# Optimization experiments

Measured on AMD Instinct MI355X. Metric: run time of the kernel, lower is better.

The kernel has to match this reference:

```python
import jax, jax.numpy as jnp
import numpy as np

B, S, D = 1, 2048, 2048
H, HKV, HD = 16, 8, 128
WINDOW = 1024
EPS = 1e-6
SCALE = HD ** -0.5


def _rope_tables(seq_len, head_dim, theta=10000.0):
    inv_freq = 1.0 / (theta ** (jnp.arange(0, head_dim, 2, dtype=jnp.float32) / head_dim))
    ang = jnp.arange(seq_len, dtype=jnp.float32)[:, None] * inv_freq[None, :]  # [S, hd/2]
    emb = jnp.concatenate([ang, ang], axis=-1)  # [S, hd]
    return jnp.cos(emb)[None], jnp.sin(emb)[None]  # [1, S, hd]


def setup_inputs() -> dict:
    key = jax.random.key(0)
    ks = jax.random.split(key, 8)
    cos, sin = _rope_tables(S, HD)
    return {
        "hidden_states": jax.random.normal(ks[0], (B, S, D), jnp.float32),
        "cos": jnp.broadcast_to(cos, (B, S, HD)),
        "sin": jnp.broadcast_to(sin, (B, S, HD)),
        "Wq": jax.random.normal(ks[1], (D, H * HD), jnp.float32) * (D ** -0.5),
        "Wk": jax.random.normal(ks[2], (D, HKV * HD), jnp.float32) * (D ** -0.5),
        "Wv": jax.random.normal(ks[3], (D, HKV * HD), jnp.float32) * (D ** -0.5),
        "Wo": jax.random.normal(ks[4], (H * HD, D), jnp.float32) * ((H * HD) ** -0.5),
        "q_scale": jax.random.uniform(ks[5], (HD,), jnp.float32, 0.5, 1.5),
        "k_scale": jax.random.uniform(ks[6], (HD,), jnp.float32, 0.5, 1.5),
    }


def _rms_norm(x, scale):
    # per-head RMSNorm over last dim, computed in fp32 (matches RMSNorm module)
    xf = x.astype(jnp.float32)
    var = jnp.mean(xf * xf, axis=-1, keepdims=True)
    return (xf * jax.lax.rsqrt(var + EPS) * scale).astype(x.dtype)


def _rotate_half(x):
    x1, x2 = x[..., : HD // 2], x[..., HD // 2 :]
    return jnp.concatenate([-x2, x1], axis=-1)


def _apply_rope(x, cos, sin):
    # cos/sin: [B,S,hd] -> [B,S,1,hd] (unsqueeze_dim=2)
    c, s = cos[:, :, None, :], sin[:, :, None, :]
    return x * c + _rotate_half(x) * s


def reference(hidden_states, cos, sin, Wq, Wk, Wv, Wo, q_scale, k_scale):
    b, s, _ = hidden_states.shape
    q = (hidden_states @ Wq).reshape(b, s, H, HD)
    k = (hidden_states @ Wk).reshape(b, s, HKV, HD)
    v = (hidden_states @ Wv).reshape(b, s, HKV, HD)
    q = _rms_norm(q, q_scale)
    k = _rms_norm(k, k_scale)
    q = _apply_rope(q, cos, sin)
    k = _apply_rope(k, cos, sin)
    # GQA: repeat kv heads to match query heads (groups are consecutive)
    g = H // HKV
    k = jnp.repeat(k, g, axis=2)  # [b, s, H, hd]
    v = jnp.repeat(v, g, axis=2)
    scores = jnp.einsum("bqhd,bkhd->bhqk", q, k) * SCALE  # [b,H,S,S]
    i = jnp.arange(s)[:, None]
    j = jnp.arange(s)[None, :]
    allowed = (j <= i) & (i - j <= WINDOW)  # causal + sliding window
    scores = jnp.where(allowed[None, None], scores, -jnp.inf)
    attn = jax.nn.softmax(scores, axis=-1)
    out = jnp.einsum("bhqk,bkhd->bqhd", attn, v).reshape(b, s, H * HD)
    return out @ Wo
```

## Files before the change

### kernel.cpp

```cpp
#include <hip/hip_runtime.h>
#include <hip/hip_bf16.h>
#include <cmath>


typedef __bf16 bf16x8 __attribute__((ext_vector_type(8)));
typedef float  f32x4  __attribute__((ext_vector_type(4)));

#define S_LEN    2048
#define NH       16
#define NKV      8
#define HDIM     128
#define WIN      1024
#define QK_SCALE_L2E 0.12751744595f
#define RMS_EPS  1e-6f

__device__ __forceinline__ void gld16(void* lds, const void* g) {
    __builtin_amdgcn_global_load_lds(
        (const __attribute__((address_space(1))) unsigned int*)g,
        (__attribute__((address_space(3))) unsigned int*)lds, 16, 0, 0);
}

__device__ __forceinline__ unsigned short f2bu(float x) {
    __hip_bfloat16 h = __float2bfloat16(x);
    return *(unsigned short*)&h;
}

__global__ __launch_bounds__(256) void trans_cvt_kernel(
    const float* __restrict__ Wq, const float* __restrict__ Wk,
    const float* __restrict__ Wv, const float* __restrict__ Wo,
    const float* __restrict__ hs,
    __hip_bfloat16* __restrict__ WqkvT, __hip_bfloat16* __restrict__ WoT,
    __hip_bfloat16* __restrict__ hsb)
{
    __shared__ __attribute__((aligned(16))) unsigned short tile[64][72];
    int id = blockIdx.x;
    if (id >= 3072) {
        size_t i = ((size_t)(id - 3072) * 256 + threadIdx.x) * 8;
        float4 a = *(const float4*)(hs + i);
        float4 b = *(const float4*)(hs + i + 4);
        unsigned short u[8] = { f2bu(a.x), f2bu(a.y), f2bu(a.z), f2bu(a.w),
                                f2bu(b.x), f2bu(b.y), f2bu(b.z), f2bu(b.w) };
        *(uint4*)(hsb + i) = *(uint4*)u;
        return;
    }
    const float* src; __hip_bfloat16* dst; int N, kt, nt;
    if (id < 1024)      { src = Wq; dst = WqkvT;                          N = 2048; kt = id >> 5;          nt = id & 31; }
    else if (id < 1536) { src = Wk; dst = WqkvT + (size_t)2048*2048;      N = 1024; kt = (id-1024) >> 4;   nt = (id-1024) & 15; }
    else if (id < 2048) { src = Wv; dst = WqkvT + (size_t)3072*2048;      N = 1024; kt = (id-1536) >> 4;   nt = (id-1536) & 15; }
    else                { src = Wo; dst = WoT;                            N = 2048; kt = (id-2048) >> 5;   nt = (id-2048) & 31; }
    int k0 = kt * 64, n0 = nt * 64;
    int tid = threadIdx.x;
#pragma unroll
    for (int p = 0; p < 2; ++p) {
        int c = p*256 + tid; int r = c >> 3, cc = (c & 7) * 8;
        const float* s = src + (size_t)(k0 + r)*N + n0 + cc;
        float4 a = *(const float4*)s;
        float4 b = *(const float4*)(s + 4);
        unsigned short u[8] = { f2bu(a.x), f2bu(a.y), f2bu(a.z), f2bu(a.w),
                                f2bu(b.x), f2bu(b.y), f2bu(b.z), f2bu(b.w) };
        *(uint4*)&tile[r][cc] = *(uint4*)u;
    }
    __syncthreads();
#pragma unroll
    for (int p = 0; p < 2; ++p) {
        int c = p*256 + tid; int r2 = c >> 3, c2 = (c & 7) * 8;
        uint4 o;
        o.x = tile[c2+0][r2] | ((unsigned)tile[c2+1][r2] << 16);
        o.y = tile[c2+2][r2] | ((unsigned)tile[c2+3][r2] << 16);
        o.z = tile[c2+4][r2] | ((unsigned)tile[c2+5][r2] << 16);
        o.w = tile[c2+6][r2] | ((unsigned)tile[c2+7][r2] << 16);
        *(uint4*)(dst + (size_t)(n0 + r2)*2048 + k0 + c2) = o;
    }
}

template <typename OT>
__global__ __launch_bounds__(256, 2) void gemm_bt_kernel(
    const __hip_bfloat16* __restrict__ A, const __hip_bfloat16* __restrict__ BT,
    OT* __restrict__ C, int M, int N, int K)
{
    __shared__ __attribute__((aligned(16))) __hip_bfloat16 As[2][128*64];
    __shared__ __attribute__((aligned(16))) __hip_bfloat16 Bs[2][128*64];
    const int tid  = threadIdx.x;
    const int lane = tid & 63;
    const int wave = tid >> 6;
    const int quad = lane >> 4, l15 = lane & 15;
    const int m0 = blockIdx.y * 128, n0 = blockIdx.x * 128;
    const int wm = (wave >> 1) * 64, wn = (wave & 1) * 64;
    const int sw = l15 & 7;

    f32x4 acc[4][4] = {};

    auto stage = [&](int b, int k0) {
#pragma unroll
        for (int p = 0; p < 4; ++p) {
            int L = p*256 + tid;
            int r = L >> 3, s = L & 7;
            int cs = s ^ (r & 7);
            gld16((char*)&As[b][0] + L*16, A + (size_t)(m0 + r)*K + k0 + cs*8);
        }
#pragma unroll
        for (int p = 0; p < 4; ++p) {
            int L = p*256 + tid;
            int r = L >> 3, s = L & 7;
            int cs = s ^ (r & 7);
            gld16((char*)&Bs[b][0] + L*16, BT + (size_t)(n0 + r)*K + k0 + cs*8);
        }
    };

    const int NT = K >> 6;
    stage(0, 0);
    int cur = 0;
    for (int kt = 0; kt < NT; ++kt, cur ^= 1) {
        __syncthreads();
        if (kt + 1 < NT) stage(cur ^ 1, (kt + 1) << 6);
#pragma unroll
        for (int ks = 0; ks < 2; ++ks) {
            const int slot = ((ks*4 + quad) ^ sw) * 8;
            bf16x8 af[4], bfr[4];
#pragma unroll
            for (int t = 0; t < 4; ++t) {
                af[t]  = *(const bf16x8*)(&As[cur][0] + (wm + t*16 + l15)*64 + slot);
                bfr[t] = *(const bf16x8*)(&Bs[cur][0] + (wn + t*16 + l15)*64 + slot);
            }
#pragma unroll
            for (int mt = 0; mt < 4; ++mt)
#pragma unroll
                for (int nt = 0; nt < 4; ++nt)
                    acc[mt][nt] = __builtin_amdgcn_mfma_f32_16x16x32_bf16(af[mt], bfr[nt], acc[mt][nt], 0, 0, 0);
        }
    }
#pragma unroll
    for (int mt = 0; mt < 4; ++mt)
#pragma unroll
        for (int nt = 0; nt < 4; ++nt)
#pragma unroll
            for (int r = 0; r < 4; ++r) {
                int row = m0 + wm + mt*16 + quad*4 + r;
                int col = n0 + wn + nt*16 + l15;
                if constexpr (__is_same(OT, float))
                    C[(size_t)row*N + col] = acc[mt][nt][r];
                else
                    C[(size_t)row*N + col] = __float2bfloat16(acc[mt][nt][r]);
            }
}

__global__ __launch_bounds__(256) void rms_vt_kernel(
    const __hip_bfloat16* __restrict__ qkv,
    const float* __restrict__ cosb, const float* __restrict__ sinb,
    const float* __restrict__ qsc,  const float* __restrict__ ksc,
    __hip_bfloat16* __restrict__ Qn, __hip_bfloat16* __restrict__ Kn,
    __hip_bfloat16* __restrict__ Vt)
{
    __shared__ __attribute__((aligned(16))) unsigned short tile[64][72];
    int id = blockIdx.x;
    if (id >= 2048) {
        int t  = id - 2048;
        int s0 = (t & 31) * 64;
        int v0 = (t >> 5) * 64;
        int tid = threadIdx.x;
#pragma unroll
        for (int p = 0; p < 2; ++p) {
            int c = p*256 + tid; int r = c >> 3, cc = (c & 7) * 8;
            uint4 v = *(const uint4*)(qkv + (size_t)(s0 + r)*4096 + 3072 + v0 + cc);
            *(uint4*)&tile[r][cc] = v;
        }
        __syncthreads();
#pragma unroll
        for (int p = 0; p < 2; ++p) {
            int c = p*256 + tid; int r2 = c >> 3, c2 = (c & 7) * 8;
            uint4 o;
            o.x = tile[c2+0][r2] | ((unsigned)tile[c2+1][r2] << 16);
            o.y = tile[c2+2][r2] | ((unsigned)tile[c2+3][r2] << 16);
            o.z = tile[c2+4][r2] | ((unsigned)tile[c2+5][r2] << 16);
            o.w = tile[c2+6][r2] | ((unsigned)tile[c2+7][r2] << 16);
            *(uint4*)(Vt + (size_t)(v0 + r2)*2048 + s0 + c2) = o;
        }
        return;
    }
    int s = id;
    int wave = threadIdx.x >> 6, lane = threadIdx.x & 63;
    float c1 = cosb[s*128 + lane];
    float c2 = cosb[s*128 + 64 + lane];
    float s1 = sinb[s*128 + lane];
    float s2 = sinb[s*128 + 64 + lane];
    for (int u = wave; u < 24; u += 4) {
        bool isq = (u < 16);
        int h = isq ? u : u - 16;
        const __hip_bfloat16* x = qkv + (size_t)s*4096 + (isq ? h*128 : 2048 + h*128);
        float x1 = (float)x[lane], x2 = (float)x[lane + 64];
        float ss = x1*x1 + x2*x2;
#pragma unroll
        for (int off = 32; off; off >>= 1) ss += __shfl_xor(ss, off);
        float r = rsqrtf(ss * (1.0f/128.0f) + RMS_EPS);
        if (isq) r *= QK_SCALE_L2E;
        const float* sc = isq ? qsc : ksc;
        float y1 = x1 * r * sc[lane];
        float y2 = x2 * r * sc[lane + 64];
        float o1 = y1*c1 - y2*s1;
        float o2 = y2*c2 + y1*s2;
        __hip_bfloat16* dst = isq ? (Qn + (size_t)s*2048 + h*128)
                                  : (Kn + (size_t)s*1024 + h*128);
        dst[lane]      = __float2bfloat16(o1);
        dst[lane + 64] = __float2bfloat16(o2);
    }
}

__global__ __launch_bounds__(256, 2) void attn_kernel(
    const __hip_bfloat16* __restrict__ Qn,
    const __hip_bfloat16* __restrict__ Kn,
    const __hip_bfloat16* __restrict__ Vt,
    __hip_bfloat16* __restrict__ O)
{
    __shared__ __attribute__((aligned(16))) __hip_bfloat16 Ksm[2][64*128];
    __shared__ __attribute__((aligned(16))) __hip_bfloat16 Vsm[2][128*64];
    __shared__ __attribute__((aligned(16))) __hip_bfloat16 P[4][16][76];

    const int bx   = blockIdx.x;
    const int h    = bx & 15;
    const int qb   = 31 - (bx >> 4);
    const int i0   = qb * 64;
    const int hk   = h >> 1;
    const int tid  = threadIdx.x, wave = tid >> 6, lane = tid & 63;
    const int quad = lane >> 4, l15 = lane & 15;
    const int ib   = i0 + wave * 16;

    const __hip_bfloat16* Kh = Kn + hk * HDIM;
    const __hip_bfloat16* Vh = Vt + (size_t)(hk * HDIM) * 2048;

    bf16x8 qf[4];
    const __hip_bfloat16* qbase = Qn + (size_t)(ib + l15)*2048 + h*HDIM + quad*8;
#pragma unroll
    for (int kk = 0; kk < 4; ++kk) qf[kk] = *(const bf16x8*)(qbase + kk*32);

    f32x4 o[8] = {};
    float lrow[4] = {0.f, 0.f, 0.f, 0.f};

    int j_lo = i0 - WIN; if (j_lo < 0) j_lo = 0;
    const int jstart = j_lo & ~63;
    const int jend   = i0;

    auto stage = [&](int b, int j0) {
#pragma unroll
        for (int p = 0; p < 4; ++p) {
            int L = p*256 + tid;
            int r = L >> 4;
            int c = (L & 15) ^ (r & 15);
            gld16((char*)&Ksm[b][0] + L*16, Kh + (size_t)(j0 + r)*1024 + c*8);
        }
#pragma unroll
        for (int p = 0; p < 4; ++p) {
            int L = p*256 + tid;
            int dv = L >> 3;
            int c = (L & 7) ^ (dv & 7);
            gld16((char*)&Vsm[b][0] + L*16, Vh + (size_t)dv*2048 + j0 + c*8);
        }
    };

    stage(0, jstart);
    int cur = 0;
    for (int j0 = jstart; j0 <= jend; j0 += 64, cur ^= 1) {
        __syncthreads();
        if (j0 + 64 <= jend) stage(cur ^ 1, j0 + 64);

        f32x4 sacc[4] = {};
#pragma unroll
        for (int nt = 0; nt < 4; ++nt) {
            const int r = nt*16 + l15;
#pragma unroll
            for (int kk = 0; kk < 4; ++kk) {
                const int cc = (kk*4 + quad) ^ l15;
                bf16x8 kfr = *(const bf16x8*)(&Ksm[cur][0] + r*128 + cc*8);
                sacc[nt] = __builtin_amdgcn_mfma_f32_16x16x32_bf16(qf[kk], kfr, sacc[nt], 0, 0, 0);
            }
        }

        const bool need_mask = (j0 + 63 > ib) || (j0 < ib + 15 - WIN);
        if (need_mask) {
#pragma unroll
            for (int nt = 0; nt < 4; ++nt) {
                int j = j0 + nt*16 + l15;
#pragma unroll
                for (int r = 0; r < 4; ++r) {
                    int i = ib + quad*4 + r;
                    bool valid = (j <= i) && (i - j <= WIN);
                    float p = valid ? __builtin_exp2f(sacc[nt][r]) : 0.f;
                    lrow[r] += p;
                    P[wave][quad*4 + r][nt*16 + l15] = __float2bfloat16(p);
                }
            }
        } else {
#pragma unroll
            for (int nt = 0; nt < 4; ++nt)
#pragma unroll
                for (int r = 0; r < 4; ++r) {
                    float p = __builtin_exp2f(sacc[nt][r]);
                    lrow[r] += p;
                    P[wave][quad*4 + r][nt*16 + l15] = __float2bfloat16(p);
                }
        }

#pragma unroll
        for (int ks = 0; ks < 2; ++ks) {
            bf16x8 pf = *(const bf16x8*)&P[wave][l15][ks*32 + quad*8];
#pragma unroll
            for (int dt = 0; dt < 8; ++dt) {
                const int dv = dt*16 + l15;
                const int cc = (ks*4 + quad) ^ (l15 & 7);
                bf16x8 vfr = *(const bf16x8*)(&Vsm[cur][0] + dv*64 + cc*8);
                o[dt] = __builtin_amdgcn_mfma_f32_16x16x32_bf16(pf, vfr, o[dt], 0, 0, 0);
            }
        }
    }

#pragma unroll
    for (int r = 0; r < 4; ++r) {
        lrow[r] += __shfl_xor(lrow[r], 1);
        lrow[r] += __shfl_xor(lrow[r], 2);
        lrow[r] += __shfl_xor(lrow[r], 4);
        lrow[r] += __shfl_xor(lrow[r], 8);
        float inv = 1.0f / lrow[r];
        int row = ib + quad*4 + r;
#pragma unroll
        for (int dt = 0; dt < 8; ++dt)
            O[(size_t)row*2048 + h*HDIM + dt*16 + l15] = __float2bfloat16(o[dt][r] * inv);
    }
}

extern "C" void kernel_launch(void* const* d_in, const int* in_sizes, int n_in,
                              void* d_out, int out_size, void* d_ws, size_t ws_size,
                              hipStream_t stream)
{
    (void)in_sizes; (void)n_in; (void)out_size; (void)ws_size;
    const float* hs   = (const float*)d_in[0];
    const float* cosb = (const float*)d_in[1];
    const float* sinb = (const float*)d_in[2];
    const float* Wq   = (const float*)d_in[3];
    const float* Wk   = (const float*)d_in[4];
    const float* Wv   = (const float*)d_in[5];
    const float* Wo   = (const float*)d_in[6];
    const float* qs   = (const float*)d_in[7];
    const float* ks   = (const float*)d_in[8];

    char* ws = (char*)d_ws;
    __hip_bfloat16* WqkvT = (__hip_bfloat16*)(ws);
    __hip_bfloat16* WoT   = (__hip_bfloat16*)(ws + (16u << 20));
    __hip_bfloat16* QKV   = (__hip_bfloat16*)(ws + (24u << 20));
    __hip_bfloat16* Qn    = (__hip_bfloat16*)(ws + (40u << 20));
    __hip_bfloat16* Kn    = (__hip_bfloat16*)(ws + (48u << 20));
    __hip_bfloat16* Vt    = (__hip_bfloat16*)(ws + (52u << 20));
    __hip_bfloat16* hsb   = (__hip_bfloat16*)(ws + (56u << 20));
    __hip_bfloat16* AT    = (__hip_bfloat16*)(ws + (56u << 20));

    trans_cvt_kernel<<<dim3(5120), dim3(256), 0, stream>>>(Wq, Wk, Wv, Wo, hs, WqkvT, WoT, hsb);
    gemm_bt_kernel<__hip_bfloat16><<<dim3(32, 16), dim3(256), 0, stream>>>(hsb, WqkvT, QKV, 2048, 4096, 2048);
    rms_vt_kernel<<<dim3(2560), dim3(256), 0, stream>>>(QKV, cosb, sinb, qs, ks, Qn, Kn, Vt);
    attn_kernel<<<dim3(512), dim3(256), 0, stream>>>(Qn, Kn, Vt, AT);
    gemm_bt_kernel<float><<<dim3(16, 16), dim3(256), 0, stream>>>(AT, WoT, (float*)d_out, 2048, 2048, 2048);
}
```

Measured before the change: 230.2 us.

## Share K/V tiles across GQA head pair in attention; retile output projection GEMM

```diff
diff --git a/kernel.cpp b/kernel.cpp
--- a/kernel.cpp
+++ b/kernel.cpp
@@ -137,6 +137,77 @@
             for (int r = 0; r < 4; ++r) {
                 int row = m0 + wm + mt*16 + quad*4 + r;
                 int col = n0 + wn + nt*16 + l15;
+                if constexpr (__is_same(OT, float))
+                    C[(size_t)row*N + col] = acc[mt][nt][r];
+                else
+                    C[(size_t)row*N + col] = __float2bfloat16(acc[mt][nt][r]);
+            }
+}
+
+template <typename OT>
+__global__ __launch_bounds__(128, 2) void gemm_bt64_kernel(
+    const __hip_bfloat16* __restrict__ A, const __hip_bfloat16* __restrict__ BT,
+    OT* __restrict__ C, int M, int N, int K)
+{
+    __shared__ __attribute__((aligned(16))) __hip_bfloat16 As[2][128*64];
+    __shared__ __attribute__((aligned(16))) __hip_bfloat16 Bs[2][64*64];
+    const int tid  = threadIdx.x;
+    const int lane = tid & 63;
+    const int wave = tid >> 6;
+    const int quad = lane >> 4, l15 = lane & 15;
+    const int m0 = blockIdx.y * 128, n0 = blockIdx.x * 64;
+    const int wm = wave * 64;
+    const int sw = l15 & 7;
+
+    f32x4 acc[4][4] = {};
+
+    auto stage = [&](int b, int k0) {
+#pragma unroll
+        for (int p = 0; p < 8; ++p) {
+            int L = p*128 + tid;
+            int r = L >> 3, s = L & 7;
+            int cs = s ^ (r & 7);
+            gld16((char*)&As[b][0] + L*16, A + (size_t)(m0 + r)*K + k0 + cs*8);
+        }
+#pragma unroll
+        for (int p = 0; p < 4; ++p) {
+            int L = p*128 + tid;
+            int r = L >> 3, s = L & 7;
+            int cs = s ^ (r & 7);
+            gld16((char*)&Bs[b][0] + L*16, BT + (size_t)(n0 + r)*K + k0 + cs*8);
+        }
+    };
+
+    const int NT = K >> 6;
+    stage(0, 0);
+    int cur = 0;
+    for (int kt = 0; kt < NT; ++kt, cur ^= 1) {
+        __syncthreads();
+        if (kt + 1 < NT) stage(cur ^ 1, (kt + 1) << 6);
+#pragma unroll
+        for (int ks = 0; ks < 2; ++ks) {
+            const int slot = ((ks*4 + quad) ^ sw) * 8;
+            bf16x8 af[4], bfr[4];
+#pragma unroll
+            for (int t = 0; t < 4; ++t) {
+                af[t]  = *(const bf16x8*)(&As[cur][0] + (wm + t*16 + l15)*64 + slot);
+                bfr[t] = *(const bf16x8*)(&Bs[cur][0] + (t*16 + l15)*64 + slot);
+            }
+#pragma unroll
+            for (int mt = 0; mt < 4; ++mt)
+#pragma unroll
+                for (int nt = 0; nt < 4; ++nt)
+                    acc[mt][nt] = __builtin_amdgcn_mfma_f32_16x16x32_bf16(af[mt], bfr[nt], acc[mt][nt], 0, 0, 0);
+        }
+    }
+#pragma unroll
+    for (int mt = 0; mt < 4; ++mt)
+#pragma unroll
+        for (int nt = 0; nt < 4; ++nt)
+#pragma unroll
+            for (int r = 0; r < 4; ++r) {
+                int row = m0 + wm + mt*16 + quad*4 + r;
+                int col = n0 + nt*16 + l15;
                 if constexpr (__is_same(OT, float))
                     C[(size_t)row*N + col] = acc[mt][nt][r];
                 else
@@ -205,7 +276,7 @@
     }
 }
 
-__global__ __launch_bounds__(256, 2) void attn_kernel(
+__global__ __launch_bounds__(256, 1) void attn_kernel(
     const __hip_bfloat16* __restrict__ Qn,
     const __hip_bfloat16* __restrict__ Kn,
     const __hip_bfloat16* __restrict__ Vt,
@@ -213,27 +284,30 @@
 {
     __shared__ __attribute__((aligned(16))) __hip_bfloat16 Ksm[2][64*128];
     __shared__ __attribute__((aligned(16))) __hip_bfloat16 Vsm[2][128*64];
-    __shared__ __attribute__((aligned(16))) __hip_bfloat16 P[4][16][76];
+    __shared__ __attribute__((aligned(16))) __hip_bfloat16 P[4][32][76];
 
     const int bx   = blockIdx.x;
-    const int h    = bx & 15;
-    const int qb   = 31 - (bx >> 4);
+    const int hk   = bx & 7;
+    const int qb   = bx >> 3;
     const int i0   = qb * 64;
-    const int hk   = h >> 1;
     const int tid  = threadIdx.x, wave = tid >> 6, lane = tid & 63;
     const int quad = lane >> 4, l15 = lane & 15;
-    const int ib   = i0 + wave * 16;
+    const int hw   = 2*hk + (wave >> 1);
+    const int ibw  = i0 + (wave & 1) * 32;
 
     const __hip_bfloat16* Kh = Kn + hk * HDIM;
     const __hip_bfloat16* Vh = Vt + (size_t)(hk * HDIM) * 2048;
 
-    bf16x8 qf[4];
-    const __hip_bfloat16* qbase = Qn + (size_t)(ib + l15)*2048 + h*HDIM + quad*8;
-#pragma unroll
-    for (int kk = 0; kk < 4; ++kk) qf[kk] = *(const bf16x8*)(qbase + kk*32);
-
-    f32x4 o[8] = {};
-    float lrow[4] = {0.f, 0.f, 0.f, 0.f};
+    bf16x8 qf[2][4];
+#pragma unroll
+    for (int m = 0; m < 2; ++m) {
+        const __hip_bfloat16* qbase = Qn + (size_t)(ibw + m*16 + l15)*2048 + hw*HDIM + quad*8;
+#pragma unroll
+        for (int kk = 0; kk < 4; ++kk) qf[m][kk] = *(const bf16x8*)(qbase + kk*32);
+    }
+
+    f32x4 o[2][8] = {};
+    float lrow[2][4] = {};
 
     int j_lo = i0 - WIN; if (j_lo < 0) j_lo = 0;
     const int jstart = j_lo & ~63;
@@ -262,7 +336,7 @@
         __syncthreads();
         if (j0 + 64 <= jend) stage(cur ^ 1, j0 + 64);
 
-        f32x4 sacc[4] = {};
+        f32x4 sacc[2][4] = {};
 #pragma unroll
         for (int nt = 0; nt < 4; ++nt) {
             const int r = nt*16 + l15;
@@ -270,60 +344,70 @@
             for (int kk = 0; kk < 4; ++kk) {
                 const int cc = (kk*4 + quad) ^ l15;
                 bf16x8 kfr = *(const bf16x8*)(&Ksm[cur][0] + r*128 + cc*8);
-                sacc[nt] = __builtin_amdgcn_mfma_f32_16x16x32_bf16(qf[kk], kfr, sacc[nt], 0, 0, 0);
-            }
-        }
-
-        const bool need_mask = (j0 + 63 > ib) || (j0 < ib + 15 - WIN);
+                sacc[0][nt] = __builtin_amdgcn_mfma_f32_16x16x32_bf16(qf[0][kk], kfr, sacc[0][nt], 0, 0, 0);
+                sacc[1][nt] = __builtin_amdgcn_mfma_f32_16x16x32_bf16(qf[1][kk], kfr, sacc[1][nt], 0, 0, 0);
+            }
+        }
+
+        const bool need_mask = (j0 + 63 > ibw) || (j0 < ibw + 31 - WIN);
         if (need_mask) {
 #pragma unroll
-            for (int nt = 0; nt < 4; ++nt) {
-                int j = j0 + nt*16 + l15;
-#pragma unroll
-                for (int r = 0; r < 4; ++r) {
-                    int i = ib + quad*4 + r;
-                    bool valid = (j <= i) && (i - j <= WIN);
-                    float p = valid ? __builtin_exp2f(sacc[nt][r]) : 0.f;
-                    lrow[r] += p;
-                    P[wave][quad*4 + r][nt*16 + l15] = __float2bfloat16(p);
+            for (int m = 0; m < 2; ++m)
+#pragma unroll
+                for (int nt = 0; nt < 4; ++nt) {
+                    int j = j0 + nt*16 + l15;
+#pragma unroll
+                    for (int r = 0; r < 4; ++r) {
+                        int i = ibw + m*16 + quad*4 + r;
+                        bool valid = (j <= i) && (i - j <= WIN);
+                        float p = valid ? __builtin_exp2f(sacc[m][nt][r]) : 0.f;
+                        lrow[m][r] += p;
+                        P[wave][m*16 + quad*4 + r][nt*16 + l15] = __float2bfloat16(p);
+                    }
                 }
-            }
         } else {
 #pragma unroll
-            for (int nt = 0; nt < 4; ++nt)
-#pragma unroll
-                for (int r = 0; r < 4; ++r) {
-                    float p = __builtin_exp2f(sacc[nt][r]);
-                    lrow[r] += p;
-                    P[wave][quad*4 + r][nt*16 + l15] = __float2bfloat16(p);
-                }
+            for (int m = 0; m < 2; ++m)
+#pragma unroll
+                for (int nt = 0; nt < 4; ++nt)
+#pragma unroll
+                    for (int r = 0; r < 4; ++r) {
+                        float p = __builtin_exp2f(sacc[m][nt][r]);
+                        lrow[m][r] += p;
+                        P[wave][m*16 + quad*4 + r][nt*16 + l15] = __float2bfloat16(p);
+                    }
         }
 
 #pragma unroll
         for (int ks = 0; ks < 2; ++ks) {
-            bf16x8 pf = *(const bf16x8*)&P[wave][l15][ks*32 + quad*8];
+            bf16x8 pf0 = *(const bf16x8*)&P[wave][l15     ][ks*32 + quad*8];
+            bf16x8 pf1 = *(const bf16x8*)&P[wave][16 + l15][ks*32 + quad*8];
 #pragma unroll
             for (int dt = 0; dt < 8; ++dt) {
                 const int dv = dt*16 + l15;
                 const int cc = (ks*4 + quad) ^ (l15 & 7);
                 bf16x8 vfr = *(const bf16x8*)(&Vsm[cur][0] + dv*64 + cc*8);
-                o[dt] = __builtin_amdgcn_mfma_f32_16x16x32_bf16(pf, vfr, o[dt], 0, 0, 0);
-            }
-        }
-    }
-
-#pragma unroll
-    for (int r = 0; r < 4; ++r) {
-        lrow[r] += __shfl_xor(lrow[r], 1);
-        lrow[r] += __shfl_xor(lrow[r], 2);
-        lrow[r] += __shfl_xor(lrow[r], 4);
-        lrow[r] += __shfl_xor(lrow[r], 8);
-        float inv = 1.0f / lrow[r];
-        int row = ib + quad*4 + r;
-#pragma unroll
-        for (int dt = 0; dt < 8; ++dt)
-            O[(size_t)row*2048 + h*HDIM + dt*16 + l15] = __float2bfloat16(o[dt][r] * inv);
-    }
+                o[0][dt] = __builtin_amdgcn_mfma_f32_16x16x32_bf16(pf0, vfr, o[0][dt], 0, 0, 0);
+                o[1][dt] = __builtin_amdgcn_mfma_f32_16x16x32_bf16(pf1, vfr, o[1][dt], 0, 0, 0);
+            }
+        }
+    }
+
+#pragma unroll
+    for (int m = 0; m < 2; ++m)
+#pragma unroll
+        for (int r = 0; r < 4; ++r) {
+            float l = lrow[m][r];
+            l += __shfl_xor(l, 1);
+            l += __shfl_xor(l, 2);
+            l += __shfl_xor(l, 4);
+            l += __shfl_xor(l, 8);
+            float inv = 1.0f / l;
+            int row = ibw + m*16 + quad*4 + r;
+#pragma unroll
+            for (int dt = 0; dt < 8; ++dt)
+                O[(size_t)row*2048 + hw*HDIM + dt*16 + l15] = __float2bfloat16(o[m][dt][r] * inv);
+        }
 }
 
 extern "C" void kernel_launch(void* const* d_in, const int* in_sizes, int n_in,
@@ -354,6 +438,6 @@
     trans_cvt_kernel<<<dim3(5120), dim3(256), 0, stream>>>(Wq, Wk, Wv, Wo, hs, WqkvT, WoT, hsb);
     gemm_bt_kernel<__hip_bfloat16><<<dim3(32, 16), dim3(256), 0, stream>>>(hsb, WqkvT, QKV, 2048, 4096, 2048);
     rms_vt_kernel<<<dim3(2560), dim3(256), 0, stream>>>(QKV, cosb, sinb, qs, ks, Qn, Kn, Vt);
-    attn_kernel<<<dim3(512), dim3(256), 0, stream>>>(Qn, Kn, Vt, AT);
-    gemm_bt_kernel<float><<<dim3(16, 16), dim3(256), 0, stream>>>(AT, WoT, (float*)d_out, 2048, 2048, 2048);
-}
+    attn_kernel<<<dim3(256), dim3(256), 0, stream>>>(Qn, Kn, Vt, AT);
+    gemm_bt64_kernel<float><<<dim3(32, 16), dim3(128), 0, stream>>>(AT, WoT, (float*)d_out, 2048, 2048, 2048);
+}
```

Result: slower. 235.3 us (+2.2%).
